# Performance work log

Hardware: AMD Instinct MI355X
Metric: run time of the kernel (lower is better)

The kernel has to match this reference:

```python
import jax, jax.numpy as jnp
import numpy as np

B, N_NUC, N_UP, N_DOWN = 512, 16, 32, 32
N_ELEC = N_UP + N_DOWN            # 64 electrons
F = 8                             # edge feature dim (Gaussian RBF envelopes)
D = N_NUC * F                     # embedding_dim = 128 (positional electron embeddings)
L = 3                             # n_interactions
N_ATOM_TYPES = 4


def _rbf(diff):
    # diff: [..., 3] -> [..., F]; Gaussian RBF features of the interparticle distance
    d = jnp.sqrt(jnp.sum(diff * diff, axis=-1) + 1e-12)
    mu = jnp.linspace(0.0, 4.0, F, dtype=diff.dtype)
    return jnp.exp(-(d[..., None] - mu) ** 2)


def setup_inputs() -> dict:
    key = jax.random.key(0)
    ks = jax.random.split(key, 9)
    r = 2.0 * jax.random.normal(ks[0], (B, N_ELEC, 3), dtype=jnp.float32)
    R = 2.0 * jax.random.normal(ks[1], (B, N_NUC, 3), dtype=jnp.float32)
    atom_types = jax.random.randint(ks[2], (N_NUC,), 0, N_ATOM_TYPES)
    embed_table = 0.1 * jax.random.normal(ks[3], (N_ATOM_TYPES, D), dtype=jnp.float32)
    we_same = 0.1 * jax.random.normal(ks[4], (L, F, D), dtype=jnp.float32)
    we_anti = 0.1 * jax.random.normal(ks[5], (L, F, D), dtype=jnp.float32)
    we_ne = 0.1 * jax.random.normal(ks[6], (L, F, D), dtype=jnp.float32)
    w_up = 0.05 * jax.random.normal(ks[7], (L, 4 * D, D), dtype=jnp.float32)
    b_up = jnp.zeros((L, D), dtype=jnp.float32)
    return {
        'r': r, 'R': R, 'embed_table': embed_table,
        'we_same': we_same, 'we_anti': we_anti, 'we_ne': we_ne,
        'w_up': w_up, 'b_up': b_up, 'atom_types': atom_types,
    }


def reference(r, R, embed_table, we_same, we_anti, we_ne, w_up, b_up, atom_types):
    # --- molecular graph edge construction (pairwise differences + edge features) ---
    ee_feat = _rbf(r[:, :, None, :] - r[:, None, :, :])   # [B, e, e, F]
    ne_feat = _rbf(r[:, :, None, :] - R[:, None, :, :])   # [B, e, n, F]

    spin = jnp.arange(N_ELEC) >= N_UP
    eye = jnp.eye(N_ELEC, dtype=bool)
    same_m = ((spin[:, None] == spin[None, :]) & ~eye).astype(ee_feat.dtype)  # no self-interaction
    anti_m = (spin[:, None] != spin[None, :]).astype(ee_feat.dtype)
    feat_same = ee_feat * same_m[None, :, :, None]
    feat_anti = ee_feat * anti_m[None, :, :, None]

    # --- node factory: positional electron embeddings (dense scatter of ne features == reshape) ---
    x = ne_feat.reshape(ne_feat.shape[0], N_ELEC, N_NUC * F)  # [B, e, D]
    y = embed_table[atom_types]                               # [n, D] nuclei embeddings

    # --- message-passing layers ---
    for l in range(L):
        # messages = Linear(edge_feats) * sender embedding, summed over senders per receiver;
        # contract sender axis first to keep intermediates at [B, e, F, D]
        t_s = jnp.einsum('bijf,bjd->bifd', feat_same, x)
        z_s = jnp.einsum('bifd,fd->bid', t_s, we_same[l])
        t_a = jnp.einsum('bijf,bjd->bifd', feat_anti, x)
        z_a = jnp.einsum('bifd,fd->bid', t_a, we_anti[l])
        t_n = jnp.einsum('binf,nd->bifd', ne_feat, y)
        z_n = jnp.einsum('bifd,fd->bid', t_n, we_ne[l])
        upd = jnp.concatenate([x, z_s, z_a, z_n], axis=-1)    # [B, e, 4D]
        x = x + jnp.tanh(upd @ w_up[l] + b_up[l])
    return x  # final electron embeddings [B, N_ELEC, D]
```

## Files before the change

### kernel.cpp

```cpp
#include <hip/hip_runtime.h>


typedef unsigned short u16;
typedef unsigned int u32;
typedef __attribute__((ext_vector_type(8))) short short8;
typedef __attribute__((ext_vector_type(4))) float f32x4;
typedef __attribute__((ext_vector_type(4))) u32 u32x4;
typedef _Float16 h2 __attribute__((ext_vector_type(2)));

__device__ __forceinline__ u16 f2h(float f){ return __builtin_bit_cast(u16, (_Float16)f); }
__device__ __forceinline__ float h2f(u16 a){ return (float)__builtin_bit_cast(_Float16, a); }

__device__ __forceinline__ short8 rbf8(float dd){
  short8 a;
#pragma unroll
  for (int f = 0; f < 8; f++){
    float u = dd - (4.0f/7.0f)*(float)f;
    a[f] = (short)f2h(__expf(-u*u));
  }
  return a;
}

__global__ __launch_bounds__(256) void gnn_prep(
    const float* __restrict__ w_up, const float* __restrict__ we_ne,
    const float* __restrict__ embed, const int* __restrict__ atypes,
    u16* __restrict__ wsegs){
  __shared__ u16 lw[16384];
  const int blk = blockIdx.x;
  const int l = blk / 5, seg = blk % 5;
  const int tid = threadIdx.x;
  if (seg < 4){
    const float* src = w_up + (l*512 + seg*128)*128;
#pragma unroll
    for (int mm = 0; mm < 16; mm++){
      int idx = mm*1024 + tid*4;
      float4 v = *(const float4*)(src + idx);
      lw[idx+0] = f2h(v.x); lw[idx+1] = f2h(v.y);
      lw[idx+2] = f2h(v.z); lw[idx+3] = f2h(v.w);
    }
  } else {
#pragma unroll
    for (int mm = 0; mm < 16; mm++){
      int idx = mm*1024 + tid*4;
      int k = idx >> 7, dout = idx & 127;
      int n = k >> 3, f = k & 7;
      float4 ye = *(const float4*)(embed + atypes[n]*128 + dout);
      float4 wn = *(const float4*)(we_ne + (l*8 + f)*128 + dout);
      lw[idx+0] = f2h(ye.x*wn.x); lw[idx+1] = f2h(ye.y*wn.y);
      lw[idx+2] = f2h(ye.z*wn.z); lw[idx+3] = f2h(ye.w*wn.w);
    }
  }
  __syncthreads();
  u16* dst = wsegs + blk*16384;
  const int col = tid & 15, q = (tid >> 4) & 3;
#pragma unroll
  for (int m = 0; m < 8; m++){
    int slot = m*4 + (tid >> 6);
    int c = slot >> 3, nt = slot & 7;
    int kbase = c*32 + q*8;
    int dout = nt*16 + col;
    short8 vv;
#pragma unroll
    for (int jj = 0; jj < 8; jj++) vv[jj] = (short)lw[(kbase+jj)*128 + dout];
    *(short8*)(dst + m*2048 + tid*8) = vv;
  }
}

__global__ __launch_bounds__(256, 2) void gnn_main(
    const float* __restrict__ r_g, const float* __restrict__ R_g,
    const float* __restrict__ weS_g, const float* __restrict__ weA_g,
    const float* __restrict__ bup_g,
    const u16* __restrict__ wsegs,
    float* __restrict__ out)
{
  __shared__ __attribute__((aligned(16))) u16 xb[64][136];
  __shared__ __attribute__((aligned(16))) u16 zst[64][136];
  __shared__ __attribute__((aligned(16))) u16 wbuf[2][4096];

  const int tid  = threadIdx.x;
  const int b    = blockIdx.x;
  const int lane = tid & 63;
  const int w    = tid >> 6;
  const int col  = lane & 15;
  const int q    = lane >> 4;
  const int i0   = w * 16;
  const int s    = w >> 1;
  const int mrow = i0 + col;
  const int loff = (q*16 + col) * 8;

  u32x4 stg[2];
  auto stg_ld = [&](const u16* src){
#pragma unroll
    for (int m = 0; m < 2; m++) stg[m] = *(const u32x4*)(src + m*2048 + tid*8);
  };
  auto stg_st = [&](u16* dst){
#pragma unroll
    for (int m = 0; m < 2; m++) *(u32x4*)(dst + m*2048 + tid*8) = stg[m];
  };
  auto gemm_q = [&](const u16* wb, short8 a, f32x4* acc){
#pragma unroll
    for (int nt = 0; nt < 8; nt++){
      short8 bb = *(const short8*)(wb + nt*512 + loff);
      acc[nt] = __builtin_amdgcn_mfma_f32_16x16x32_f16(a, bb, acc[nt], 0, 0, 0);
    }
  };

  float dS[8], dA[8], dN[4];
  {
    float* rs = (float*)&zst[0][0];
    float* Rs = rs + 256;
    if (tid < 64){
#pragma unroll
      for (int k = 0; k < 3; k++) rs[tid*4+k] = r_g[(b*64+tid)*3 + k];
    } else if (tid < 80){
      int n = tid - 64;
#pragma unroll
      for (int k = 0; k < 3; k++) Rs[n*4+k] = R_g[(b*16+n)*3 + k];
    }
    __syncthreads();
    {
      float x0 = rs[mrow*4], x1 = rs[mrow*4+1], x2 = rs[mrow*4+2];
#pragma unroll
      for (int c = 0; c < 8; c++){
        int j = 32*s + 4*c + q;
        float dx = x0-rs[j*4], dy = x1-rs[j*4+1], dz = x2-rs[j*4+2];
        dS[c] = sqrtf(dx*dx + dy*dy + dz*dz + 1e-12f);
        j = 32*(1-s) + 4*c + q;
        dx = x0-rs[j*4]; dy = x1-rs[j*4+1]; dz = x2-rs[j*4+2];
        dA[c] = sqrtf(dx*dx + dy*dy + dz*dz + 1e-12f);
      }
#pragma unroll
      for (int c = 0; c < 4; c++){
        int n = 4*c + q;
        float dx = x0-Rs[n*4], dy = x1-Rs[n*4+1], dz = x2-Rs[n*4+2];
        dN[c] = sqrtf(dx*dx + dy*dy + dz*dz + 1e-12f);
      }
    }
    {
      int i = tid >> 2, nb = (tid & 3)*4;
      float y0 = rs[i*4], y1 = rs[i*4+1], y2 = rs[i*4+2];
#pragma unroll
      for (int nn = 0; nn < 4; nn++){
        int n = nb + nn;
        float dx = y0-Rs[n*4], dy = y1-Rs[n*4+1], dz = y2-Rs[n*4+2];
        float dd = sqrtf(dx*dx + dy*dy + dz*dz + 1e-12f);
        *(short8*)&xb[i][n*8] = rbf8(dd);
      }
    }
    stg_ld(wsegs + 0);
    stg_st(wbuf[0]);
    __syncthreads();
  }

  f32x4 xr[8];
#pragma unroll
  for (int nt = 0; nt < 8; nt++)
#pragma unroll
    for (int rr = 0; rr < 4; rr++)
      xr[nt][rr] = h2f(xb[i0 + q*4 + rr][nt*16 + col]);

  const f32x4 vzero = {0.f, 0.f, 0.f, 0.f};

#pragma unroll 1
  for (int l = 0; l < 3; l++){
    const u16* slab = wsegs + l*81920;
    float bupr[8];
#pragma unroll
    for (int nt = 0; nt < 8; nt++) bupr[nt] = bup_g[l*128 + nt*16 + col];

    f32x4 upd[8], zn[8];
#pragma unroll
    for (int nt = 0; nt < 8; nt++){ upd[nt] = vzero; zn[nt] = vzero; }

    auto zpass = [&](int pass){
      const float* weX = pass ? weA_g : weS_g;
      const int jb0 = pass ? 32*(1-s) : 32*s;
      const float* dX = pass ? dA : dS;
      h2 wp[8][4];
#pragma unroll
      for (int nt = 0; nt < 8; nt++)
#pragma unroll
        for (int p = 0; p < 4; p++){
          h2 t;
          t[0] = (_Float16)weX[(l*8 + 2*p  )*128 + nt*16 + col];
          t[1] = (_Float16)weX[(l*8 + 2*p+1)*128 + nt*16 + col];
          wp[nt][p] = t;
        }
      short8 aF[8];
#pragma unroll
      for (int c = 0; c < 8; c++){
        aF[c] = rbf8(dX[c]);
        if (!pass && (jb0 + 4*c + q == mrow)) aF[c] = (short8)0;
      }
      f32x4 zacc[8];
#pragma unroll
      for (int nt = 0; nt < 8; nt++) zacc[nt] = vzero;
#pragma unroll
      for (int nt = 0; nt < 8; nt++){
        u16 xv[8];
#pragma unroll
        for (int c = 0; c < 8; c++) xv[c] = xb[jb0 + 4*c + q][nt*16 + col];
#pragma unroll
        for (int c = 0; c < 8; c++){
          _Float16 xh = __builtin_bit_cast(_Float16, xv[c]);
          h2 xd; xd[0] = xh; xd[1] = xh;
          u32x4 bu;
#pragma unroll
          for (int p = 0; p < 4; p++)
            bu[p] = __builtin_bit_cast(u32, (h2)(xd * wp[nt][p]));
          short8 bb = __builtin_bit_cast(short8, bu);
          zacc[nt] = __builtin_amdgcn_mfma_f32_16x16x32_f16(aF[c], bb, zacc[nt], 0, 0, 0);
        }
      }
#pragma unroll
      for (int nt = 0; nt < 8; nt++)
#pragma unroll
        for (int rr = 0; rr < 4; rr++)
          zst[i0 + q*4 + rr][nt*16 + col] = f2h(zacc[nt][rr]);
    };

    auto A_xb  = [&](int c){ return *(const short8*)&xb [mrow][c*32 + (q<<3)]; };
    auto A_zst = [&](int c){ return *(const short8*)&zst[mrow][c*32 + (q<<3)]; };
    const u16* const sl = slab;
#define QP(seg,c) (sl + (seg)*16384 + (c)*4096)
#define PHASE(nxt, pc, afrag, acc) \
    { stg_ld(nxt); gemm_q(wbuf[pc], (afrag), (acc)); stg_st(wbuf[1-(pc)]); __syncthreads(); }

    stg_ld(QP(0,1)); zpass(0);
    gemm_q(wbuf[0], A_xb(0), upd);
    stg_st(wbuf[1]); __syncthreads();
    PHASE(QP(0,2), 1, A_xb(1), upd)
    PHASE(QP(0,3), 0, A_xb(2), upd)
    PHASE(QP(1,0), 1, A_xb(3), upd)
    PHASE(QP(1,1), 0, A_zst(0), upd)
    PHASE(QP(1,2), 1, A_zst(1), upd)
    PHASE(QP(1,3), 0, A_zst(2), upd)
    stg_ld(QP(2,0));
    gemm_q(wbuf[1], A_zst(3), upd);
    zpass(1);
    stg_st(wbuf[0]); __syncthreads();
    PHASE(QP(2,1), 0, A_zst(0), upd)
    PHASE(QP(2,2), 1, A_zst(1), upd)
    PHASE(QP(2,3), 0, A_zst(2), upd)
    PHASE(QP(4,0), 1, A_zst(3), upd)
    PHASE(QP(4,1), 0, rbf8(dN[0]), zn)
    PHASE(QP(4,2), 1, rbf8(dN[1]), zn)
    PHASE(QP(4,3), 0, rbf8(dN[2]), zn)
    stg_ld(QP(3,0));
    gemm_q(wbuf[1], rbf8(dN[3]), zn);
#pragma unroll
    for (int nt = 0; nt < 8; nt++)
#pragma unroll
      for (int rr = 0; rr < 4; rr++)
        zst[i0 + q*4 + rr][nt*16 + col] = f2h(zn[nt][rr]);
    stg_st(wbuf[0]); __syncthreads();
    PHASE(QP(3,1), 0, A_zst(0), upd)
    PHASE(QP(3,2), 1, A_zst(1), upd)
    PHASE(QP(3,3), 0, A_zst(2), upd)
    if (l < 2) stg_ld(sl + 81920);
    gemm_q(wbuf[1], A_zst(3), upd);
#pragma unroll
    for (int nt = 0; nt < 8; nt++){
#pragma unroll
      for (int rr = 0; rr < 4; rr++){
        float v = upd[nt][rr] + bupr[nt];
        float e = __expf(2.0f * v);
        float th = 1.0f - 2.0f * __builtin_amdgcn_rcpf(e + 1.0f);
        xr[nt][rr] += th;
      }
    }
    if (l < 2){
      stg_st(wbuf[0]);
#pragma unroll
      for (int nt = 0; nt < 8; nt++)
#pragma unroll
        for (int rr = 0; rr < 4; rr++)
          xb[i0 + q*4 + rr][nt*16 + col] = f2h(xr[nt][rr]);
      __syncthreads();
    } else {
#pragma unroll
      for (int nt = 0; nt < 8; nt++)
#pragma unroll
        for (int rr = 0; rr < 4; rr++)
          out[(b*64 + i0 + q*4 + rr)*128 + nt*16 + col] = xr[nt][rr];
    }
#undef QP
#undef PHASE
  }
}

extern "C" void kernel_launch(void* const* d_in, const int* in_sizes, int n_in,
                              void* d_out, int out_size, void* d_ws, size_t ws_size,
                              hipStream_t stream){
  const float* r     = (const float*)d_in[0];
  const float* R     = (const float*)d_in[1];
  const float* embed = (const float*)d_in[2];
  const float* weS   = (const float*)d_in[3];
  const float* weA   = (const float*)d_in[4];
  const float* weN   = (const float*)d_in[5];
  const float* wup   = (const float*)d_in[6];
  const float* bup   = (const float*)d_in[7];
  const int* atyp    = (const int*)d_in[8];

  u16* wsegs = (u16*)d_ws;

  gnn_prep<<<15, 256, 0, stream>>>(wup, weN, embed, atyp, wsegs);
  gnn_main<<<512, 256, 0, stream>>>(r, R, weS, weA, bup, wsegs, (float*)d_out);
}
```

Before: 137.0 us.

## Process two batch items per block sharing full weight segments in LDS

Each block now handles two molecules with 512 threads, so each staged weight segment in LDS is reused by both. Weights are staged a whole 128x128 segment at a time instead of quarter chunks, which cuts the number of barriers per layer from about twenty to five. RBF A-fragments for the electron-electron pairs are now computed once before the layer loop and kept in registers. In exchange the block uses about 132KB of dynamic LDS and register pressure rises, which may lower occupancy, and only 256 blocks are launched.

```diff
diff --git a/kernel.cpp b/kernel.cpp
--- a/kernel.cpp
+++ b/kernel.cpp
@@ -66,54 +66,67 @@
   }
 }
 
-__global__ __launch_bounds__(256, 2) void gnn_main(
+__global__ __launch_bounds__(512, 2) void gnn_main(
     const float* __restrict__ r_g, const float* __restrict__ R_g,
     const float* __restrict__ weS_g, const float* __restrict__ weA_g,
     const float* __restrict__ bup_g,
     const u16* __restrict__ wsegs,
     float* __restrict__ out)
 {
-  __shared__ __attribute__((aligned(16))) u16 xb[64][136];
-  __shared__ __attribute__((aligned(16))) u16 zst[64][136];
-  __shared__ __attribute__((aligned(16))) u16 wbuf[2][4096];
+  extern __shared__ __attribute__((aligned(16))) u16 lds[];
+  u16* const wb0 = lds;
+  u16* const wb1 = lds + 16384;
+  u16* const xbB = lds + 32768;
+  u16* const zsB = lds + 50176;
 
   const int tid  = threadIdx.x;
-  const int b    = blockIdx.x;
   const int lane = tid & 63;
   const int w    = tid >> 6;
+  const int bb   = w >> 2;
+  const int wq   = w & 3;
+  const int b    = blockIdx.x*2 + bb;
   const int col  = lane & 15;
   const int q    = lane >> 4;
-  const int i0   = w * 16;
-  const int s    = w >> 1;
+  const int i0   = wq * 16;
+  const int sp   = wq >> 1;
   const int mrow = i0 + col;
   const int loff = (q*16 + col) * 8;
 
-  u32x4 stg[2];
+  u16* const xb  = xbB + bb*8704;
+  u16* const zst = zsB + bb*8704;
+
+  u32x4 stg[4];
   auto stg_ld = [&](const u16* src){
 #pragma unroll
-    for (int m = 0; m < 2; m++) stg[m] = *(const u32x4*)(src + m*2048 + tid*8);
+    for (int m = 0; m < 4; m++) stg[m] = *(const u32x4*)(src + m*4096 + tid*8);
   };
   auto stg_st = [&](u16* dst){
 #pragma unroll
-    for (int m = 0; m < 2; m++) *(u32x4*)(dst + m*2048 + tid*8) = stg[m];
+    for (int m = 0; m < 4; m++) *(u32x4*)(dst + m*4096 + tid*8) = stg[m];
   };
-  auto gemm_q = [&](const u16* wb, short8 a, f32x4* acc){
-#pragma unroll
-    for (int nt = 0; nt < 8; nt++){
-      short8 bb = *(const short8*)(wb + nt*512 + loff);
-      acc[nt] = __builtin_amdgcn_mfma_f32_16x16x32_f16(a, bb, acc[nt], 0, 0, 0);
+  auto gemm_seg = [&](const u16* wbuf, const u16* arows, f32x4* acc){
+#pragma unroll
+    for (int c = 0; c < 4; c++){
+      short8 a = *(const short8*)(arows + mrow*136 + c*32 + (q<<3));
+#pragma unroll
+      for (int nt = 0; nt < 8; nt++){
+        short8 bf = *(const short8*)(wbuf + c*4096 + nt*512 + loff);
+        acc[nt] = __builtin_amdgcn_mfma_f32_16x16x32_f16(a, bf, acc[nt], 0, 0, 0);
+      }
     }
   };
 
-  float dS[8], dA[8], dN[4];
+  short8 aS[8], aA[8];
+  float dN[4];
   {
-    float* rs = (float*)&zst[0][0];
+    float* rs = (float*)(zsB + bb*8704);
     float* Rs = rs + 256;
-    if (tid < 64){
-#pragma unroll
-      for (int k = 0; k < 3; k++) rs[tid*4+k] = r_g[(b*64+tid)*3 + k];
-    } else if (tid < 80){
-      int n = tid - 64;
+    const int ht = tid & 255;
+    if (ht < 64){
+#pragma unroll
+      for (int k = 0; k < 3; k++) rs[ht*4+k] = r_g[(b*64+ht)*3 + k];
+    } else if (ht < 80){
+      int n = ht - 64;
 #pragma unroll
       for (int k = 0; k < 3; k++) Rs[n*4+k] = R_g[(b*16+n)*3 + k];
     }
@@ -122,12 +135,14 @@
       float x0 = rs[mrow*4], x1 = rs[mrow*4+1], x2 = rs[mrow*4+2];
 #pragma unroll
       for (int c = 0; c < 8; c++){
-        int j = 32*s + 4*c + q;
+        int j = 32*sp + 4*c + q;
         float dx = x0-rs[j*4], dy = x1-rs[j*4+1], dz = x2-rs[j*4+2];
-        dS[c] = sqrtf(dx*dx + dy*dy + dz*dz + 1e-12f);
-        j = 32*(1-s) + 4*c + q;
+        float dd = sqrtf(dx*dx + dy*dy + dz*dz + 1e-12f);
+        aS[c] = rbf8(dd);
+        if (j == mrow) aS[c] = (short8)0;
+        j = 32*(1-sp) + 4*c + q;
         dx = x0-rs[j*4]; dy = x1-rs[j*4+1]; dz = x2-rs[j*4+2];
-        dA[c] = sqrtf(dx*dx + dy*dy + dz*dz + 1e-12f);
+        aA[c] = rbf8(sqrtf(dx*dx + dy*dy + dz*dz + 1e-12f));
       }
 #pragma unroll
       for (int c = 0; c < 4; c++){
@@ -137,18 +152,18 @@
       }
     }
     {
-      int i = tid >> 2, nb = (tid & 3)*4;
+      int i = (tid & 255) >> 2, nb = (tid & 3)*4;
       float y0 = rs[i*4], y1 = rs[i*4+1], y2 = rs[i*4+2];
 #pragma unroll
       for (int nn = 0; nn < 4; nn++){
         int n = nb + nn;
         float dx = y0-Rs[n*4], dy = y1-Rs[n*4+1], dz = y2-Rs[n*4+2];
         float dd = sqrtf(dx*dx + dy*dy + dz*dz + 1e-12f);
-        *(short8*)&xb[i][n*8] = rbf8(dd);
+        *(short8*)&xb[i*136 + n*8] = rbf8(dd);
       }
     }
     stg_ld(wsegs + 0);
-    stg_st(wbuf[0]);
+    stg_st(wb0);
     __syncthreads();
   }
 
@@ -157,49 +172,45 @@
   for (int nt = 0; nt < 8; nt++)
 #pragma unroll
     for (int rr = 0; rr < 4; rr++)
-      xr[nt][rr] = h2f(xb[i0 + q*4 + rr][nt*16 + col]);
+      xr[nt][rr] = h2f(xb[(i0 + q*4 + rr)*136 + nt*16 + col]);
 
   const f32x4 vzero = {0.f, 0.f, 0.f, 0.f};
 
 #pragma unroll 1
   for (int l = 0; l < 3; l++){
     const u16* slab = wsegs + l*81920;
+    const int P = l & 1;
+    u16* const bufA = P ? wb1 : wb0;
+    u16* const bufB = P ? wb0 : wb1;
+
     float bupr[8];
 #pragma unroll
     for (int nt = 0; nt < 8; nt++) bupr[nt] = bup_g[l*128 + nt*16 + col];
 
-    f32x4 upd[8], zn[8];
-#pragma unroll
-    for (int nt = 0; nt < 8; nt++){ upd[nt] = vzero; zn[nt] = vzero; }
+    f32x4 upd[8];
+#pragma unroll
+    for (int nt = 0; nt < 8; nt++) upd[nt] = vzero;
 
     auto zpass = [&](int pass){
       const float* weX = pass ? weA_g : weS_g;
-      const int jb0 = pass ? 32*(1-s) : 32*s;
-      const float* dX = pass ? dA : dS;
-      h2 wp[8][4];
-#pragma unroll
-      for (int nt = 0; nt < 8; nt++)
+      const int jb0 = pass ? 32*(1-sp) : 32*sp;
+      const short8* aF = pass ? aA : aS;
+      f32x4 zacc[8];
+#pragma unroll
+      for (int nt = 0; nt < 8; nt++) zacc[nt] = vzero;
+#pragma unroll
+      for (int nt = 0; nt < 8; nt++){
+        h2 wp[4];
 #pragma unroll
         for (int p = 0; p < 4; p++){
           h2 t;
           t[0] = (_Float16)weX[(l*8 + 2*p  )*128 + nt*16 + col];
           t[1] = (_Float16)weX[(l*8 + 2*p+1)*128 + nt*16 + col];
-          wp[nt][p] = t;
+          wp[p] = t;
         }
-      short8 aF[8];
-#pragma unroll
-      for (int c = 0; c < 8; c++){
-        aF[c] = rbf8(dX[c]);
-        if (!pass && (jb0 + 4*c + q == mrow)) aF[c] = (short8)0;
-      }
-      f32x4 zacc[8];
-#pragma unroll
-      for (int nt = 0; nt < 8; nt++) zacc[nt] = vzero;
-#pragma unroll
-      for (int nt = 0; nt < 8; nt++){
         u16 xv[8];
 #pragma unroll
-        for (int c = 0; c < 8; c++) xv[c] = xb[jb0 + 4*c + q][nt*16 + col];
+        for (int c = 0; c < 8; c++) xv[c] = xb[(jb0 + 4*c + q)*136 + nt*16 + col];
 #pragma unroll
         for (int c = 0; c < 8; c++){
           _Float16 xh = __builtin_bit_cast(_Float16, xv[c]);
@@ -207,58 +218,52 @@
           u32x4 bu;
 #pragma unroll
           for (int p = 0; p < 4; p++)
-            bu[p] = __builtin_bit_cast(u32, (h2)(xd * wp[nt][p]));
-          short8 bb = __builtin_bit_cast(short8, bu);
-          zacc[nt] = __builtin_amdgcn_mfma_f32_16x16x32_f16(aF[c], bb, zacc[nt], 0, 0, 0);
+            bu[p] = __builtin_bit_cast(u32, (h2)(xd * wp[p]));
+          short8 bf = __builtin_bit_cast(short8, bu);
+          zacc[nt] = __builtin_amdgcn_mfma_f32_16x16x32_f16(aF[c], bf, zacc[nt], 0, 0, 0);
         }
       }
 #pragma unroll
       for (int nt = 0; nt < 8; nt++)
 #pragma unroll
         for (int rr = 0; rr < 4; rr++)
-          zst[i0 + q*4 + rr][nt*16 + col] = f2h(zacc[nt][rr]);
+          zst[(i0 + q*4 + rr)*136 + nt*16 + col] = f2h(zacc[nt][rr]);
     };
 
-    auto A_xb  = [&](int c){ return *(const short8*)&xb [mrow][c*32 + (q<<3)]; };
-    auto A_zst = [&](int c){ return *(const short8*)&zst[mrow][c*32 + (q<<3)]; };
-    const u16* const sl = slab;
-#define QP(seg,c) (sl + (seg)*16384 + (c)*4096)
-#define PHASE(nxt, pc, afrag, acc) \
-    { stg_ld(nxt); gemm_q(wbuf[pc], (afrag), (acc)); stg_st(wbuf[1-(pc)]); __syncthreads(); }
-
-    stg_ld(QP(0,1)); zpass(0);
-    gemm_q(wbuf[0], A_xb(0), upd);
-    stg_st(wbuf[1]); __syncthreads();
-    PHASE(QP(0,2), 1, A_xb(1), upd)
-    PHASE(QP(0,3), 0, A_xb(2), upd)
-    PHASE(QP(1,0), 1, A_xb(3), upd)
-    PHASE(QP(1,1), 0, A_zst(0), upd)
-    PHASE(QP(1,2), 1, A_zst(1), upd)
-    PHASE(QP(1,3), 0, A_zst(2), upd)
-    stg_ld(QP(2,0));
-    gemm_q(wbuf[1], A_zst(3), upd);
+    stg_ld(slab + 1*16384);
+    zpass(0);
+    gemm_seg(bufA, xb, upd);
+    stg_st(bufB); __syncthreads();
+    stg_ld(slab + 2*16384);
+    gemm_seg(bufB, zst, upd);
+    stg_st(bufA); __syncthreads();
+    stg_ld(slab + 4*16384);
     zpass(1);
-    stg_st(wbuf[0]); __syncthreads();
-    PHASE(QP(2,1), 0, A_zst(0), upd)
-    PHASE(QP(2,2), 1, A_zst(1), upd)
-    PHASE(QP(2,3), 0, A_zst(2), upd)
-    PHASE(QP(4,0), 1, A_zst(3), upd)
-    PHASE(QP(4,1), 0, rbf8(dN[0]), zn)
-    PHASE(QP(4,2), 1, rbf8(dN[1]), zn)
-    PHASE(QP(4,3), 0, rbf8(dN[2]), zn)
-    stg_ld(QP(3,0));
-    gemm_q(wbuf[1], rbf8(dN[3]), zn);
-#pragma unroll
-    for (int nt = 0; nt < 8; nt++)
-#pragma unroll
-      for (int rr = 0; rr < 4; rr++)
-        zst[i0 + q*4 + rr][nt*16 + col] = f2h(zn[nt][rr]);
-    stg_st(wbuf[0]); __syncthreads();
-    PHASE(QP(3,1), 0, A_zst(0), upd)
-    PHASE(QP(3,2), 1, A_zst(1), upd)
-    PHASE(QP(3,3), 0, A_zst(2), upd)
-    if (l < 2) stg_ld(sl + 81920);
-    gemm_q(wbuf[1], A_zst(3), upd);
+    gemm_seg(bufA, zst, upd);
+    stg_st(bufB); __syncthreads();
+    stg_ld(slab + 3*16384);
+    {
+      f32x4 zn[8];
+#pragma unroll
+      for (int nt = 0; nt < 8; nt++) zn[nt] = vzero;
+#pragma unroll
+      for (int c = 0; c < 4; c++){
+        short8 a = rbf8(dN[c]);
+#pragma unroll
+        for (int nt = 0; nt < 8; nt++){
+          short8 bf = *(const short8*)(bufB + c*4096 + nt*512 + loff);
+          zn[nt] = __builtin_amdgcn_mfma_f32_16x16x32_f16(a, bf, zn[nt], 0, 0, 0);
+        }
+      }
+#pragma unroll
+      for (int nt = 0; nt < 8; nt++)
+#pragma unroll
+        for (int rr = 0; rr < 4; rr++)
+          zst[(i0 + q*4 + rr)*136 + nt*16 + col] = f2h(zn[nt][rr]);
+    }
+    stg_st(bufA); __syncthreads();
+    if (l < 2) stg_ld(slab + 81920);
+    gemm_seg(bufA, zst, upd);
 #pragma unroll
     for (int nt = 0; nt < 8; nt++){
 #pragma unroll
@@ -270,12 +275,12 @@
       }
     }
     if (l < 2){
-      stg_st(wbuf[0]);
 #pragma unroll
       for (int nt = 0; nt < 8; nt++)
 #pragma unroll
         for (int rr = 0; rr < 4; rr++)
-          xb[i0 + q*4 + rr][nt*16 + col] = f2h(xr[nt][rr]);
+          xb[(i0 + q*4 + rr)*136 + nt*16 + col] = f2h(xr[nt][rr]);
+      stg_st(bufB);
       __syncthreads();
     } else {
 #pragma unroll
@@ -284,8 +289,6 @@
         for (int rr = 0; rr < 4; rr++)
           out[(b*64 + i0 + q*4 + rr)*128 + nt*16 + col] = xr[nt][rr];
     }
-#undef QP
-#undef PHASE
   }
 }
 
@@ -304,6 +307,8 @@
 
   u16* wsegs = (u16*)d_ws;
 
+  (void)hipFuncSetAttribute((const void*)gnn_main,
+                            hipFuncAttributeMaxDynamicSharedMemorySize, 135168);
   gnn_prep<<<15, 256, 0, stream>>>(wup, weN, embed, atyp, wsegs);
-  gnn_main<<<512, 256, 0, stream>>>(r, R, weS, weA, bup, wsegs, (float*)d_out);
+  gnn_main<<<256, 512, 135168, stream>>>(r, R, weS, weA, bup, wsegs, (float*)d_out);
 }
```

New measurement: 136.4 us. No clear change (-0.5%).
